# Performance work log

Measured on AMD Instinct MI355X. Metric: run time of the kernel, lower is better.

## Reference

```python
import jax, jax.numpy as jnp
import numpy as np

EMBED_DIM = 512
NUM_HEADS = 8
HEAD_DIM = EMBED_DIM // NUM_HEADS
EDGE_HIDDEN = 512
B, L = 2, 512


def setup_inputs() -> dict:
    key = jax.random.key(0)
    ks = jax.random.split(key, 16)
    s = 0.02
    inp = {
        "query": jax.random.normal(ks[0], (B, L, EMBED_DIM), jnp.float32),
        "key_in": jax.random.normal(ks[1], (B, L, EMBED_DIM), jnp.float32),
        "value": jax.random.normal(ks[2], (B, L, EMBED_DIM), jnp.float32),
        "edge_representation": jax.random.normal(ks[3], (B, L, L), jnp.float32),
        # projection weights stored as [in, out]: y = x @ W + b
        "Wq": jax.random.normal(ks[4], (EMBED_DIM, EMBED_DIM), jnp.float32) * s,
        "bq": jnp.zeros((EMBED_DIM,), jnp.float32),
        "Wk": jax.random.normal(ks[5], (EMBED_DIM, EMBED_DIM), jnp.float32) * s,
        "bk": jnp.zeros((EMBED_DIM,), jnp.float32),
        "Wv": jax.random.normal(ks[6], (EMBED_DIM, EMBED_DIM), jnp.float32) * s,
        "bv": jnp.zeros((EMBED_DIM,), jnp.float32),
        "Wo": jax.random.normal(ks[7], (EMBED_DIM, EMBED_DIM), jnp.float32) * s,
        "bo": jnp.zeros((EMBED_DIM,), jnp.float32),
        # edge MLP: Linear(1 -> 512) -> ReLU -> Linear(512 -> num_heads)
        "We1": jax.random.normal(ks[8], (1, EDGE_HIDDEN), jnp.float32) * s,
        "be1": jnp.zeros((EDGE_HIDDEN,), jnp.float32),
        "We2": jax.random.normal(ks[9], (EDGE_HIDDEN, NUM_HEADS), jnp.float32) * s,
        "be2": jnp.zeros((NUM_HEADS,), jnp.float32),
    }
    return inp


def reference(query, key_in, value, edge_representation,
              Wq, bq, Wk, bk, Wv, bv, Wo, bo, We1, be1, We2, be2):
    Bc, Lc, _ = query.shape
    # project and split heads: [B, H, L, Dh]
    def split_heads(x):
        return x.reshape(Bc, Lc, NUM_HEADS, HEAD_DIM).transpose(0, 2, 1, 3)
    Q = split_heads(query @ Wq + bq)
    K = split_heads(key_in @ Wk + bk)
    V = split_heads(value @ Wv + bv)
    # edge MLP on scalar edge features: [B, L, L, 1] -> [B, L, L, H]
    e = edge_representation[..., None]
    h = jax.nn.relu(e * We1[0] + be1)          # [B, L, L, 512]
    edge_bias = h @ We2 + be2                   # [B, L, L, H]
    scale = 1.0 / jnp.sqrt(jnp.asarray(HEAD_DIM, query.dtype))
    scores = jnp.einsum("bhqd,bhkd->bhqk", Q, K) * scale
    scores = scores + edge_bias.transpose(0, 3, 1, 2)  # [B, H, L, L]
    attn = jax.nn.softmax(scores, axis=-1)
    out = jnp.einsum("bhqk,bhkd->bhqd", attn, V)
    out = out.transpose(0, 2, 1, 3).reshape(Bc, Lc, EMBED_DIM)
    return out @ Wo + bo
```

## Files before the change

kernel.cpp:

```cpp
#include <hip/hip_runtime.h>
#include <hip/hip_bf16.h>

typedef __attribute__((ext_vector_type(8))) short bf16x8;
typedef __attribute__((ext_vector_type(4))) float f32x4;

#define LOG2E 1.44269504088896340736f

#define QB_OFF 2621440
#define KB_OFF 3145728
#define VT_OFF 3670016
#define AO_OFF 4194304
#define T_B   9437184
#define A_B   (T_B + 4096)
#define C_B   (A_B + 20480)

struct MegaArgs {
  const float *xq, *xk, *xv, *eg;
  const float *wq, *wk, *wv, *wo;
  const float *bq, *bk, *bv, *bo;
  const float *w1, *b1, *we2, *be2;
  float* out;
  unsigned short* wsb;
  float *wsT, *wsA, *wsC;
};

__device__ __forceinline__ unsigned short f2bf(float f) {
  union { __hip_bfloat16 h; unsigned short u; } c;
  c.h = __float2bfloat16(f);
  return c.u;
}

__device__ __forceinline__ uint4 pack8(float4 a, float4 b) {
  union { unsigned short us[8]; uint4 u; } r;
  r.us[0] = f2bf(a.x); r.us[1] = f2bf(a.y); r.us[2] = f2bf(a.z); r.us[3] = f2bf(a.w);
  r.us[4] = f2bf(b.x); r.us[5] = f2bf(b.y); r.us[6] = f2bf(b.z); r.us[7] = f2bf(b.w);
  return r.u;
}

__device__ void prep_block(const MegaArgs& a, char* smem) {
  float* sT   = (float*)smem;
  int*   sIdx = (int*)(smem + 2048);
  float (*sDA)[8] = (float (*)[8])(smem + 4096);
  float (*sDC)[8] = (float (*)[8])(smem + 20480);
  float* sA0 = (float*)(smem + 36864);
  float* sC0 = (float*)(smem + 36896);
  int tid = threadIdx.x, lane = tid & 63, w = tid >> 6;
  float accA[8] = {0,0,0,0,0,0,0,0}, accC[8] = {0,0,0,0,0,0,0,0};
  for (int e = 0; e < 2; ++e) {
    int p = tid + e * 256;
    float ww = a.w1[p], bb = a.b1[p];
    sT[p] = (ww != 0.f) ? (-bb / ww) : -3.4e38f;
    sIdx[p] = p;
#pragma unroll
    for (int h = 0; h < 8; ++h) {
      float w2 = a.we2[p * 8 + h];
      if (ww < 0.f)       { accA[h] += w2 * ww; accC[h] += w2 * bb; }
      else if (ww == 0.f) { accC[h] += w2 * fmaxf(bb, 0.f); }
    }
  }
  __syncthreads();
  for (int size = 2; size <= 512; size <<= 1) {
    for (int stride = size >> 1; stride > 0; stride >>= 1) {
      if (size >= 256 && stride >= 64) __syncthreads();
      else __builtin_amdgcn_wave_barrier();
      int p = tid;
      int i = ((p / stride) * (stride << 1)) + (p % stride);
      int j = i + stride;
      bool up = ((i & size) == 0);
      float ti = sT[i], tj = sT[j];
      if (up ? (ti > tj) : (ti < tj)) {
        sT[i] = tj; sT[j] = ti;
        int t = sIdx[i]; sIdx[i] = sIdx[j]; sIdx[j] = t;
      }
    }
  }
  for (int off = 32; off > 0; off >>= 1) {
#pragma unroll
    for (int h = 0; h < 8; ++h) {
      accA[h] += __shfl_xor(accA[h], off);
      accC[h] += __shfl_xor(accC[h], off);
    }
  }
  if (lane == 0) {
#pragma unroll
    for (int h = 0; h < 8; ++h) { sDA[w][h] = accA[h]; sDC[w][h] = accC[h]; }
  }
  __syncthreads();
  if (tid < 8) {
    sA0[tid] = sDA[0][tid] + sDA[1][tid] + sDA[2][tid] + sDA[3][tid];
    sC0[tid] = sDC[0][tid] + sDC[1][tid] + sDC[2][tid] + sDC[3][tid] + a.be2[tid];
  }
  __syncthreads();
  for (int e = 0; e < 2; ++e) {
    int p = tid + e * 256;
    int k = sIdx[p];
    float wk = a.w1[k], bk2 = a.b1[k];
#pragma unroll
    for (int h = 0; h < 8; ++h) {
      float w2 = a.we2[k * 8 + h];
      float da = 0.f, dc = 0.f;
      if (wk > 0.f)      { da =  w2 * wk; dc =  w2 * bk2; }
      else if (wk < 0.f) { da = -w2 * wk; dc = -w2 * bk2; }
      sDA[p][h] = da; sDC[p][h] = dc;
    }
  }
  __syncthreads();
  for (int off = 1; off < 512; off <<= 1) {
    float ra[2][8], rc[2][8];
#pragma unroll
    for (int e = 0; e < 2; ++e) {
      int p = tid + e * 256;
      if (p >= off) {
#pragma unroll
        for (int h = 0; h < 8; ++h) { ra[e][h] = sDA[p - off][h]; rc[e][h] = sDC[p - off][h]; }
      }
    }
    __syncthreads();
#pragma unroll
    for (int e = 0; e < 2; ++e) {
      int p = tid + e * 256;
      if (p >= off) {
#pragma unroll
        for (int h = 0; h < 8; ++h) { sDA[p][h] += ra[e][h]; sDC[p][h] += rc[e][h]; }
      }
    }
    __syncthreads();
  }
  bool n0 = (tid == 0) || (sT[tid] != sT[tid - 1]);
  bool n1 = (sT[tid + 256] != sT[tid + 255]);
  unsigned long long m0 = __ballot(n0), m1 = __ballot(n1);
  unsigned long long below = (1ull << lane) - 1ull;
  int loc0 = __popcll(m0 & below), loc1 = __popcll(m1 & below);
  int* tot = sIdx;
  if (lane == 0) { tot[w] = __popcll(m0); tot[4 + w] = __popcll(m1); }
  __syncthreads();
  int t[8];
#pragma unroll
  for (int j = 0; j < 8; ++j) t[j] = tot[j];
  int nuniq = t[0] + t[1] + t[2] + t[3] + t[4] + t[5] + t[6] + t[7];
  int off0 = 0, off1 = t[0] + t[1] + t[2] + t[3];
  for (int j = 0; j < 4; ++j) {
    if (j < w) { off0 += t[j]; off1 += t[4 + j]; }
  }
  if (n0) {
    int u = off0 + loc0;
    a.wsT[u] = sT[tid];
    if (tid == 0) {
#pragma unroll
      for (int h = 0; h < 8; ++h) { a.wsA[h * 513] = sA0[h]; a.wsC[h * 513] = sC0[h]; }
    } else {
#pragma unroll
      for (int h = 0; h < 8; ++h) {
        a.wsA[h * 513 + u] = sA0[h] + sDA[tid - 1][h];
        a.wsC[h * 513 + u] = sC0[h] + sDC[tid - 1][h];
      }
    }
  }
  if (n1) {
    int u = off1 + loc1;
    a.wsT[u] = sT[tid + 256];
#pragma unroll
    for (int h = 0; h < 8; ++h) {
      a.wsA[h * 513 + u] = sA0[h] + sDA[tid + 255][h];
      a.wsC[h * 513 + u] = sC0[h] + sDC[tid + 255][h];
    }
  }
  if (tid == 0) {
#pragma unroll
    for (int h = 0; h < 8; ++h) {
      a.wsA[h * 513 + nuniq] = sA0[h] + sDA[511][h];
      a.wsC[h * 513 + nuniq] = sC0[h] + sDC[511][h];
    }
    *(int*)(a.wsT + 512) = nuniq;
  }
}

__device__ void gemm_core(const float* __restrict__ Af, const unsigned short* __restrict__ Ab,
                          const float* __restrict__ W, const float* __restrict__ bias,
                          void* out, int mode, int m0, int n0, char* smem) {
  unsigned short (*sA)[72]  = (unsigned short (*)[72])smem;
  unsigned short (*sBt)[72] = (unsigned short (*)[72])(smem + 9216);
  int tid = threadIdx.x, wave = tid >> 6, lane = tid & 63;
  int quad = lane >> 4, l16 = lane & 15;
  f32x4 acc[4] = {{0.f,0.f,0.f,0.f},{0.f,0.f,0.f,0.f},{0.f,0.f,0.f,0.f},{0.f,0.f,0.f,0.f}};
  int lr = tid >> 2, ls = tid & 3;
  int kb8 = lr >> 3, klo = lr & 7;
  for (int kb = 0; kb < 512; kb += 64) {
    __syncthreads();
    if (Af) {
      const float4* ap = (const float4*)(Af + (size_t)(m0 + lr) * 512 + kb + ls * 16);
      float4 v0 = ap[0], v1 = ap[1], v2 = ap[2], v3 = ap[3];
      *(uint4*)&sA[lr][ls * 16]     = pack8(v0, v1);
      *(uint4*)&sA[lr][ls * 16 + 8] = pack8(v2, v3);
    } else {
      *(uint4*)&sA[lr][ls * 16]     = *(const uint4*)(Ab + (size_t)(m0 + lr) * 512 + kb + ls * 16);
      *(uint4*)&sA[lr][ls * 16 + 8] = *(const uint4*)(Ab + (size_t)(m0 + lr) * 512 + kb + ls * 16 + 8);
    }
    {
      const float4* wp = (const float4*)(W + (size_t)(kb + lr) * 512 + n0 + ls * 16);
      float4 w0 = wp[0], w1 = wp[1], w2 = wp[2], w3 = wp[3];
      int nb = ls * 16;
      int slot = ((kb8 ^ ls) << 3) + klo;
      sBt[nb + 0][slot] = f2bf(w0.x);  sBt[nb + 1][slot] = f2bf(w0.y);
      sBt[nb + 2][slot] = f2bf(w0.z);  sBt[nb + 3][slot] = f2bf(w0.w);
      sBt[nb + 4][slot] = f2bf(w1.x);  sBt[nb + 5][slot] = f2bf(w1.y);
      sBt[nb + 6][slot] = f2bf(w1.z);  sBt[nb + 7][slot] = f2bf(w1.w);
      sBt[nb + 8][slot] = f2bf(w2.x);  sBt[nb + 9][slot] = f2bf(w2.y);
      sBt[nb + 10][slot] = f2bf(w2.z); sBt[nb + 11][slot] = f2bf(w2.w);
      sBt[nb + 12][slot] = f2bf(w3.x); sBt[nb + 13][slot] = f2bf(w3.y);
      sBt[nb + 14][slot] = f2bf(w3.z); sBt[nb + 15][slot] = f2bf(w3.w);
    }
    __syncthreads();
    for (int ks = 0; ks < 2; ++ks) {
      bf16x8 af = *(const bf16x8*)&sA[wave * 16 + l16][ks * 32 + quad * 8];
#pragma unroll
      for (int nt = 0; nt < 4; ++nt) {
        bf16x8 bf = *(const bf16x8*)&sBt[nt * 16 + l16][((ks * 4 + quad) ^ nt) * 8];
        acc[nt] = __builtin_amdgcn_mfma_f32_16x16x32_bf16(af, bf, acc[nt], 0, 0, 0);
      }
    }
  }
  int mbase = m0 + wave * 16 + quad * 4;
#pragma unroll
  for (int nt = 0; nt < 4; ++nt) {
    int n = n0 + nt * 16 + l16;
    float bv = bias[n];
#pragma unroll
    for (int r = 0; r < 4; ++r) {
      float v = acc[nt][r] + bv;
      int m = mbase + r;
      if (mode == 0) {
        int b = m >> 9, l = m & 511, hh = n >> 6, d = n & 63;
        ((unsigned short*)out)[(((size_t)(b * 8 + hh) * 512) + l) * 64 + d] = f2bf(v);
      } else if (mode == 1) {
        ((float*)out)[(size_t)m * 512 + n] = v;
      } else {
        int b = m >> 9, l = m & 511, hh = n >> 6, d = n & 63;
        ((unsigned short*)out)[(((size_t)(b * 8 + hh) * 64) + d) * 512 + l] = f2bf(v);
      }
    }
  }
}

__device__ void attn_block(const MegaArgs& a, int qt, int h, int b, char* smem) {
  float* sT  = (float*)smem;
  float* sAh = (float*)(smem + 2048);
  float* sCh = (float*)(smem + 4100);
  unsigned short (*sP)[16][40] = (unsigned short (*)[16][40])(smem + 6160);
  float (*sO)[4][16][16] = (float (*)[4][16][16])(smem + 11280);
  float (*sM)[16] = (float (*)[16])(smem + 27664);
  float (*sL)[16] = (float (*)[16])(smem + 27920);
  const unsigned short* Qb = a.wsb + QB_OFF;
  const unsigned short* Kb = a.wsb + KB_OFF;
  const unsigned short* Vt = a.wsb + VT_OFF;
  int bh = b * 8 + h;
  int q0 = qt * 16;
  int tid = threadIdx.x, wave = tid >> 6, lane = tid & 63;
  int quad = lane >> 4, l16 = lane & 15;
  int nu = *(const int*)(a.wsT + 512);
  for (int i = tid; i < nu; i += 256) sT[i] = a.wsT[i];
  for (int i = tid; i <= nu; i += 256) { sAh[i] = a.wsA[h * 513 + i]; sCh[i] = a.wsC[h * 513 + i]; }
  const unsigned short* qp = Qb + ((size_t)bh * 512 + q0 + l16) * 64 + quad * 8;
  bf16x8 qf0 = *(const bf16x8*)qp;
  bf16x8 qf1 = *(const bf16x8*)(qp + 32);
  int key_base = wave * 128;
  f32x4 S[4][2];
#pragma unroll
  for (int kt = 0; kt < 4; ++kt) {
    int key0 = key_base + kt * 32;
#pragma unroll
    for (int half = 0; half < 2; ++half) {
      const unsigned short* kp = Kb + ((size_t)bh * 512 + key0 + half * 16 + l16) * 64 + quad * 8;
      bf16x8 kf0 = *(const bf16x8*)kp;
      bf16x8 kf1 = *(const bf16x8*)(kp + 32);
      f32x4 acc = {0.f, 0.f, 0.f, 0.f};
      acc = __builtin_amdgcn_mfma_f32_16x16x32_bf16(qf0, kf0, acc, 0, 0, 0);
      acc = __builtin_amdgcn_mfma_f32_16x16x32_bf16(qf1, kf1, acc, 0, 0, 0);
      S[kt][half] = acc;
    }
  }
  __syncthreads();
#pragma unroll
  for (int kt = 0; kt < 4; ++kt)
#pragma unroll
    for (int half = 0; half < 2; ++half)
#pragma unroll
      for (int r = 0; r < 4; ++r) {
        int eidx = (b * 512 + q0 + quad * 4 + r) * 512 + key_base + kt * 32 + half * 16 + l16;
        float ev = a.eg[eidx];
        int lo = 0, hi = nu;
        while (lo < hi) {
          int mid = (lo + hi) >> 1;
          bool c = sT[mid] < ev;
          lo = c ? mid + 1 : lo;
          hi = c ? hi : mid;
        }
        S[kt][half][r] = S[kt][half][r] * 0.125f + sAh[lo] * ev + sCh[lo];
      }
  float m_w[4], l_w[4];
#pragma unroll
  for (int r = 0; r < 4; ++r) {
    float mx = -3.4e38f;
#pragma unroll
    for (int kt = 0; kt < 4; ++kt) { mx = fmaxf(mx, fmaxf(S[kt][0][r], S[kt][1][r])); }
    for (int off = 1; off < 16; off <<= 1) mx = fmaxf(mx, __shfl_xor(mx, off, 64));
    float s = 0.f;
#pragma unroll
    for (int kt = 0; kt < 4; ++kt)
#pragma unroll
      for (int half = 0; half < 2; ++half) {
        float p = exp2f((S[kt][half][r] - mx) * LOG2E);
        S[kt][half][r] = p; s += p;
      }
    for (int off = 1; off < 16; off <<= 1) s += __shfl_xor(s, off, 64);
    m_w[r] = mx; l_w[r] = s;
  }
  f32x4 Oacc[4] = {{0.f,0.f,0.f,0.f},{0.f,0.f,0.f,0.f},{0.f,0.f,0.f,0.f},{0.f,0.f,0.f,0.f}};
#pragma unroll
  for (int kt = 0; kt < 4; ++kt) {
    int key0 = key_base + kt * 32;
#pragma unroll
    for (int half = 0; half < 2; ++half)
#pragma unroll
      for (int r = 0; r < 4; ++r)
        sP[wave][quad * 4 + r][half * 16 + l16] = f2bf(S[kt][half][r]);
    __builtin_amdgcn_wave_barrier();
    bf16x8 pf = *(const bf16x8*)&sP[wave][l16][quad * 8];
    __builtin_amdgcn_wave_barrier();
#pragma unroll
    for (int nt = 0; nt < 4; ++nt) {
      bf16x8 vf = *(const bf16x8*)(Vt + ((size_t)bh * 64 + nt * 16 + l16) * 512 + key0 + quad * 8);
      Oacc[nt] = __builtin_amdgcn_mfma_f32_16x16x32_bf16(pf, vf, Oacc[nt], 0, 0, 0);
    }
  }
  if (l16 == 0) {
#pragma unroll
    for (int r = 0; r < 4; ++r) { sM[wave][quad * 4 + r] = m_w[r]; sL[wave][quad * 4 + r] = l_w[r]; }
  }
#pragma unroll
  for (int nt = 0; nt < 4; ++nt)
#pragma unroll
    for (int r = 0; r < 4; ++r)
      sO[wave][nt][quad * 4 + r][l16] = Oacc[nt][r];
  __syncthreads();
#pragma unroll
  for (int r = 0; r < 4; ++r) {
    int row = quad * 4 + r;
    float M = fmaxf(fmaxf(sM[0][row], sM[1][row]), fmaxf(sM[2][row], sM[3][row]));
    float L = 0.f, Ov = 0.f;
#pragma unroll
    for (int wv = 0; wv < 4; ++wv) {
      float f = exp2f((sM[wv][row] - M) * LOG2E);
      L += f * sL[wv][row];
      Ov += f * sO[wv][wave][row][l16];
    }
    float v = Ov / L;
    (a.wsb + AO_OFF)[((size_t)(b * 512 + q0 + row)) * 512 + h * 64 + wave * 16 + l16] = f2bf(v);
  }
}

__global__ __launch_bounds__(256) void k1(MegaArgs a) {
  __shared__ __align__(16) char smem[36928];
  int blk = blockIdx.x;
  if (blk == 0) {
    prep_block(a, smem);
  } else {
    int g = blk - 1, z = g >> 7, rem = g & 127;
    const float* A    = (z == 0) ? a.xq : (z == 1) ? a.xk : a.xv;
    const float* W    = (z == 0) ? a.wq : (z == 1) ? a.wk : a.wv;
    const float* bias = (z == 0) ? a.bq : (z == 1) ? a.bk : a.bv;
    void* outp = (void*)(a.wsb + ((z == 0) ? QB_OFF : (z == 1) ? KB_OFF : VT_OFF));
    gemm_core(A, nullptr, W, bias, outp, (z == 2) ? 2 : 0, (rem & 15) * 64, (rem >> 4) * 64, smem);
  }
}

__global__ __launch_bounds__(256) void k2(MegaArgs a) {
  __shared__ __align__(16) char smem[28176];
  int blk = blockIdx.x;
  attn_block(a, blk & 31, (blk >> 5) & 7, blk >> 8, smem);
}

__global__ __launch_bounds__(256) void k3(MegaArgs a) {
  __shared__ __align__(16) char smem[18432];
  gemm_core(nullptr, a.wsb + AO_OFF, a.wo, a.bo, (void*)a.out, 1,
            (blockIdx.x & 15) * 64, (blockIdx.x >> 4) * 64, smem);
}

extern "C" void kernel_launch(void* const* d_in, const int* in_sizes, int n_in,
                              void* d_out, int out_size, void* d_ws, size_t ws_size,
                              hipStream_t stream) {
  MegaArgs a;
  a.xq  = (const float*)d_in[0];
  a.xk  = (const float*)d_in[1];
  a.xv  = (const float*)d_in[2];
  a.eg  = (const float*)d_in[3];
  a.wq  = (const float*)d_in[4];
  a.bq  = (const float*)d_in[5];
  a.wk  = (const float*)d_in[6];
  a.bk  = (const float*)d_in[7];
  a.wv  = (const float*)d_in[8];
  a.bv  = (const float*)d_in[9];
  a.wo  = (const float*)d_in[10];
  a.bo  = (const float*)d_in[11];
  a.w1  = (const float*)d_in[12];
  a.b1  = (const float*)d_in[13];
  a.we2 = (const float*)d_in[14];
  a.be2 = (const float*)d_in[15];
  a.out = (float*)d_out;
  a.wsb = (unsigned short*)d_ws;
  a.wsT = (float*)((char*)d_ws + T_B);
  a.wsA = (float*)((char*)d_ws + A_B);
  a.wsC = (float*)((char*)d_ws + C_B);

  k1<<<385, 256, 0, stream>>>(a);
  k2<<<512, 256, 0, stream>>>(a);
  k3<<<128, 256, 0, stream>>>(a);
}
```

Before: 137.9 us.

## Pre-convert activations and transposed weights to bf16, load GEMM tiles directly to LDS

Adds a prep kernel that converts the Q/K/V inputs to bf16 and transposes all four weight matrices into bf16 [n,k] layout in workspace. The projection GEMMs then stage tiles with global_load_lds into XOR-swizzled LDS, with no per-element conversion or scattered transposed stores in the main loop. The attention grid index mapping is also reordered so heads vary fastest. The cost is an extra kernel launch and an extra round trip of the activations and weights through global memory.

```diff
diff --git a/kernel.cpp b/kernel.cpp
--- a/kernel.cpp
+++ b/kernel.cpp
@@ -13,6 +13,8 @@
 #define T_B   9437184
 #define A_B   (T_B + 4096)
 #define C_B   (A_B + 20480)
+#define XB_OFF 8388608
+#define WT_OFF 9961472
 
 struct MegaArgs {
   const float *xq, *xk, *xv, *eg;
@@ -35,6 +37,12 @@
   r.us[0] = f2bf(a.x); r.us[1] = f2bf(a.y); r.us[2] = f2bf(a.z); r.us[3] = f2bf(a.w);
   r.us[4] = f2bf(b.x); r.us[5] = f2bf(b.y); r.us[6] = f2bf(b.z); r.us[7] = f2bf(b.w);
   return r.u;
+}
+
+__device__ __forceinline__ void gload16(const void* g, void* l) {
+  __builtin_amdgcn_global_load_lds(
+      (const __attribute__((address_space(1))) unsigned int*)g,
+      (__attribute__((address_space(3))) unsigned int*)l, 16, 0, 0);
 }
 
 __device__ void prep_block(const MegaArgs& a, char* smem) {
@@ -175,47 +183,69 @@
   }
 }
 
-__device__ void gemm_core(const float* __restrict__ Af, const unsigned short* __restrict__ Ab,
-                          const float* __restrict__ W, const float* __restrict__ bias,
-                          void* out, int mode, int m0, int n0, char* smem) {
-  unsigned short (*sA)[72]  = (unsigned short (*)[72])smem;
-  unsigned short (*sBt)[72] = (unsigned short (*)[72])(smem + 9216);
+__device__ void xconv_block(const float* __restrict__ x, unsigned short* __restrict__ xb, int j) {
+  int tid = threadIdx.x;
+  size_t base = (size_t)j * 16384;
+#pragma unroll
+  for (int it = 0; it < 8; ++it) {
+    size_t idx = base + it * 2048 + tid * 8;
+    float4 va = *(const float4*)(x + idx);
+    float4 vb = *(const float4*)(x + idx + 4);
+    *(uint4*)(xb + idx) = pack8(va, vb);
+  }
+}
+
+__device__ void wtrans_block(const float* __restrict__ W, unsigned short* __restrict__ Wt,
+                             int tile, char* smem) {
+  float (*sW)[65] = (float (*)[65])smem;
+  int tid = threadIdx.x;
+  int k0 = (tile >> 3) * 64, n0 = (tile & 7) * 64;
+  int kr = tid >> 4, c4 = (tid & 15) * 4;
+#pragma unroll
+  for (int p = 0; p < 4; ++p) {
+    int k = p * 16 + kr;
+    float4 v = *(const float4*)(W + (size_t)(k0 + k) * 512 + n0 + c4);
+    sW[k][c4] = v.x; sW[k][c4 + 1] = v.y; sW[k][c4 + 2] = v.z; sW[k][c4 + 3] = v.w;
+  }
+  __syncthreads();
+  int n = tid >> 3, kk = (tid & 7) * 8;
+#pragma unroll
+  for (int p = 0; p < 2; ++p) {
+    int nn = p * 32 + n;
+    float4 va, vb;
+    va.x = sW[kk][nn];     va.y = sW[kk + 1][nn]; va.z = sW[kk + 2][nn]; va.w = sW[kk + 3][nn];
+    vb.x = sW[kk + 4][nn]; vb.y = sW[kk + 5][nn]; vb.z = sW[kk + 6][nn]; vb.w = sW[kk + 7][nn];
+    *(uint4*)(Wt + (size_t)(n0 + nn) * 512 + k0 + kk) = pack8(va, vb);
+  }
+}
+
+__device__ void gemm_bf(const unsigned short* __restrict__ A,
+                        const unsigned short* __restrict__ Bt,
+                        const float* __restrict__ bias,
+                        void* out, int mode, int m0, int n0, char* smem) {
+  char* sA = smem;
+  char* sB = smem + 8192;
   int tid = threadIdx.x, wave = tid >> 6, lane = tid & 63;
   int quad = lane >> 4, l16 = lane & 15;
+  int lg = lane & 7, lr8 = lane >> 3;
   f32x4 acc[4] = {{0.f,0.f,0.f,0.f},{0.f,0.f,0.f,0.f},{0.f,0.f,0.f,0.f},{0.f,0.f,0.f,0.f}};
-  int lr = tid >> 2, ls = tid & 3;
-  int kb8 = lr >> 3, klo = lr & 7;
+  int swr = l16 & 7;
   for (int kb = 0; kb < 512; kb += 64) {
     __syncthreads();
-    if (Af) {
-      const float4* ap = (const float4*)(Af + (size_t)(m0 + lr) * 512 + kb + ls * 16);
-      float4 v0 = ap[0], v1 = ap[1], v2 = ap[2], v3 = ap[3];
-      *(uint4*)&sA[lr][ls * 16]     = pack8(v0, v1);
-      *(uint4*)&sA[lr][ls * 16 + 8] = pack8(v2, v3);
-    } else {
-      *(uint4*)&sA[lr][ls * 16]     = *(const uint4*)(Ab + (size_t)(m0 + lr) * 512 + kb + ls * 16);
-      *(uint4*)&sA[lr][ls * 16 + 8] = *(const uint4*)(Ab + (size_t)(m0 + lr) * 512 + kb + ls * 16 + 8);
-    }
-    {
-      const float4* wp = (const float4*)(W + (size_t)(kb + lr) * 512 + n0 + ls * 16);
-      float4 w0 = wp[0], w1 = wp[1], w2 = wp[2], w3 = wp[3];
-      int nb = ls * 16;
-      int slot = ((kb8 ^ ls) << 3) + klo;
-      sBt[nb + 0][slot] = f2bf(w0.x);  sBt[nb + 1][slot] = f2bf(w0.y);
-      sBt[nb + 2][slot] = f2bf(w0.z);  sBt[nb + 3][slot] = f2bf(w0.w);
-      sBt[nb + 4][slot] = f2bf(w1.x);  sBt[nb + 5][slot] = f2bf(w1.y);
-      sBt[nb + 6][slot] = f2bf(w1.z);  sBt[nb + 7][slot] = f2bf(w1.w);
-      sBt[nb + 8][slot] = f2bf(w2.x);  sBt[nb + 9][slot] = f2bf(w2.y);
-      sBt[nb + 10][slot] = f2bf(w2.z); sBt[nb + 11][slot] = f2bf(w2.w);
-      sBt[nb + 12][slot] = f2bf(w3.x); sBt[nb + 13][slot] = f2bf(w3.y);
-      sBt[nb + 14][slot] = f2bf(w3.z); sBt[nb + 15][slot] = f2bf(w3.w);
+#pragma unroll
+    for (int p = 0; p < 2; ++p) {
+      int row = (p * 4 + wave) * 8 + lr8;
+      int swz = (lg ^ lr8) << 3;
+      gload16(A  + (size_t)(m0 + row) * 512 + kb + swz, sA + ((p * 4 + wave) << 10));
+      gload16(Bt + (size_t)(n0 + row) * 512 + kb + swz, sB + ((p * 4 + wave) << 10));
     }
     __syncthreads();
+#pragma unroll
     for (int ks = 0; ks < 2; ++ks) {
-      bf16x8 af = *(const bf16x8*)&sA[wave * 16 + l16][ks * 32 + quad * 8];
+      bf16x8 af = *(const bf16x8*)(sA + (wave * 16 + l16) * 128 + (((ks * 4 + quad) ^ swr) << 4));
 #pragma unroll
       for (int nt = 0; nt < 4; ++nt) {
-        bf16x8 bf = *(const bf16x8*)&sBt[nt * 16 + l16][((ks * 4 + quad) ^ nt) * 8];
+        bf16x8 bf = *(const bf16x8*)(sB + (nt * 16 + l16) * 128 + (((ks * 4 + quad) ^ swr) << 4));
         acc[nt] = __builtin_amdgcn_mfma_f32_16x16x32_bf16(af, bf, acc[nt], 0, 0, 0);
       }
     }
@@ -359,31 +389,42 @@
   }
 }
 
-__global__ __launch_bounds__(256) void k1(MegaArgs a) {
+__global__ __launch_bounds__(256) void kprep(MegaArgs a) {
   __shared__ __align__(16) char smem[36928];
   int blk = blockIdx.x;
-  if (blk == 0) {
-    prep_block(a, smem);
-  } else {
-    int g = blk - 1, z = g >> 7, rem = g & 127;
-    const float* A    = (z == 0) ? a.xq : (z == 1) ? a.xk : a.xv;
-    const float* W    = (z == 0) ? a.wq : (z == 1) ? a.wk : a.wv;
-    const float* bias = (z == 0) ? a.bq : (z == 1) ? a.bk : a.bv;
-    void* outp = (void*)(a.wsb + ((z == 0) ? QB_OFF : (z == 1) ? KB_OFF : VT_OFF));
-    gemm_core(A, nullptr, W, bias, outp, (z == 2) ? 2 : 0, (rem & 15) * 64, (rem >> 4) * 64, smem);
-  }
-}
-
-__global__ __launch_bounds__(256) void k2(MegaArgs a) {
+  if (blk == 0) { prep_block(a, smem); return; }
+  if (blk <= 96) {
+    int g = blk - 1, z = g >> 5, j = g & 31;
+    const float* x = (z == 0) ? a.xq : (z == 1) ? a.xk : a.xv;
+    xconv_block(x, a.wsb + XB_OFF + (size_t)z * 524288, j);
+    return;
+  }
+  int g = blk - 97, z = g >> 6, t = g & 63;
+  const float* W = (z == 0) ? a.wq : (z == 1) ? a.wk : (z == 2) ? a.wv : a.wo;
+  wtrans_block(W, a.wsb + WT_OFF + (size_t)z * 262144, t, smem);
+}
+
+__global__ __launch_bounds__(256) void kqkv(MegaArgs a) {
+  __shared__ __align__(16) char smem[16384];
+  int blk = blockIdx.x;
+  int z = blk >> 7, rem = blk & 127;
+  const unsigned short* A  = a.wsb + XB_OFF + (size_t)z * 524288;
+  const unsigned short* Bt = a.wsb + WT_OFF + (size_t)z * 262144;
+  const float* bias = (z == 0) ? a.bq : (z == 1) ? a.bk : a.bv;
+  void* outp = (void*)(a.wsb + ((z == 0) ? QB_OFF : (z == 1) ? KB_OFF : VT_OFF));
+  gemm_bf(A, Bt, bias, outp, (z == 2) ? 2 : 0, (rem & 15) * 64, (rem >> 4) * 64, smem);
+}
+
+__global__ __launch_bounds__(256) void kattn(MegaArgs a) {
   __shared__ __align__(16) char smem[28176];
   int blk = blockIdx.x;
-  attn_block(a, blk & 31, (blk >> 5) & 7, blk >> 8, smem);
-}
-
-__global__ __launch_bounds__(256) void k3(MegaArgs a) {
-  __shared__ __align__(16) char smem[18432];
-  gemm_core(nullptr, a.wsb + AO_OFF, a.wo, a.bo, (void*)a.out, 1,
-            (blockIdx.x & 15) * 64, (blockIdx.x >> 4) * 64, smem);
+  attn_block(a, (blk >> 3) & 31, blk & 7, blk >> 8, smem);
+}
+
+__global__ __launch_bounds__(256) void kout(MegaArgs a) {
+  __shared__ __align__(16) char smem[16384];
+  gemm_bf(a.wsb + AO_OFF, a.wsb + WT_OFF + (size_t)3 * 262144, a.bo, (void*)a.out, 1,
+          (blockIdx.x & 15) * 64, (blockIdx.x >> 4) * 64, smem);
 }
 
 extern "C" void kernel_launch(void* const* d_in, const int* in_sizes, int n_in,
@@ -412,7 +453,8 @@
   a.wsA = (float*)((char*)d_ws + A_B);
   a.wsC = (float*)((char*)d_ws + C_B);
 
-  k1<<<385, 256, 0, stream>>>(a);
-  k2<<<512, 256, 0, stream>>>(a);
-  k3<<<128, 256, 0, stream>>>(a);
-}
+  kprep<<<353, 256, 0, stream>>>(a);
+  kqkv<<<384, 256, 0, stream>>>(a);
+  kattn<<<512, 256, 0, stream>>>(a);
+  kout<<<128, 256, 0, stream>>>(a);
+}
```

After: 145.3 us. 1.05x slower.

## Fuse three kernels into one persistent kernel with grid-wide barriers

Applied to the files above, without the earlier changes.

Replaces the three launches (QKV projection, attention, output projection) with one persistent kernel of 256 blocks that loops over the work of each stage and separates the stages with atomic-counter grid barriers. A memset of the barrier counters is added before the launch. The aim is to remove kernel launch gaps and tail effects between stages. In exchange each block now runs two attention tiles serially, fewer blocks run in each stage, and the spin barriers add their own cost. Correctness depends on all 256 blocks being co-resident on the GPU.

```diff
diff --git a/kernel.cpp b/kernel.cpp
--- a/kernel.cpp
+++ b/kernel.cpp
@@ -13,6 +13,8 @@
 #define T_B   9437184
 #define A_B   (T_B + 4096)
 #define C_B   (A_B + 20480)
+#define BAR_B 16777216
+#define NBLK  256
 
 struct MegaArgs {
   const float *xq, *xk, *xv, *eg;
@@ -35,6 +37,19 @@
   r.us[0] = f2bf(a.x); r.us[1] = f2bf(a.y); r.us[2] = f2bf(a.z); r.us[3] = f2bf(a.w);
   r.us[4] = f2bf(b.x); r.us[5] = f2bf(b.y); r.us[6] = f2bf(b.z); r.us[7] = f2bf(b.w);
   return r.u;
+}
+
+__device__ __forceinline__ void gbar(unsigned int* cnt) {
+  __syncthreads();
+  if (threadIdx.x == 0) {
+    __threadfence();
+    __hip_atomic_fetch_add(cnt, 1u, __ATOMIC_RELEASE, __HIP_MEMORY_SCOPE_AGENT);
+    while (__hip_atomic_load(cnt, __ATOMIC_ACQUIRE, __HIP_MEMORY_SCOPE_AGENT) < NBLK) {
+      __builtin_amdgcn_s_sleep(8);
+    }
+    __threadfence();
+  }
+  __syncthreads();
 }
 
 __device__ void prep_block(const MegaArgs& a, char* smem) {
@@ -359,31 +374,44 @@
   }
 }
 
-__global__ __launch_bounds__(256) void k1(MegaArgs a) {
+__global__ __launch_bounds__(256) void kfused(MegaArgs a) {
   __shared__ __align__(16) char smem[36928];
+  unsigned int* bar = (unsigned int*)((char*)a.wsb + BAR_B);
   int blk = blockIdx.x;
+
   if (blk == 0) {
     prep_block(a, smem);
   } else {
-    int g = blk - 1, z = g >> 7, rem = g & 127;
-    const float* A    = (z == 0) ? a.xq : (z == 1) ? a.xk : a.xv;
-    const float* W    = (z == 0) ? a.wq : (z == 1) ? a.wk : a.wv;
-    const float* bias = (z == 0) ? a.bq : (z == 1) ? a.bk : a.bv;
-    void* outp = (void*)(a.wsb + ((z == 0) ? QB_OFF : (z == 1) ? KB_OFF : VT_OFF));
-    gemm_core(A, nullptr, W, bias, outp, (z == 2) ? 2 : 0, (rem & 15) * 64, (rem >> 4) * 64, smem);
-  }
-}
-
-__global__ __launch_bounds__(256) void k2(MegaArgs a) {
-  __shared__ __align__(16) char smem[28176];
-  int blk = blockIdx.x;
-  attn_block(a, blk & 31, (blk >> 5) & 7, blk >> 8, smem);
-}
-
-__global__ __launch_bounds__(256) void k3(MegaArgs a) {
-  __shared__ __align__(16) char smem[18432];
-  gemm_core(nullptr, a.wsb + AO_OFF, a.wo, a.bo, (void*)a.out, 1,
-            (blockIdx.x & 15) * 64, (blockIdx.x >> 4) * 64, smem);
+    int g = blk - 1;
+    for (int rep = 0; rep < 2; ++rep) {
+      if (g < 384) {
+        int z = g >> 7, rem = g & 127;
+        const float* A    = (z == 0) ? a.xq : (z == 1) ? a.xk : a.xv;
+        const float* W    = (z == 0) ? a.wq : (z == 1) ? a.wk : a.wv;
+        const float* bias = (z == 0) ? a.bq : (z == 1) ? a.bk : a.bv;
+        void* outp = (void*)(a.wsb + ((z == 0) ? QB_OFF : (z == 1) ? KB_OFF : VT_OFF));
+        gemm_core(A, nullptr, W, bias, outp, (z == 2) ? 2 : 0,
+                  (rem & 15) * 64, (rem >> 4) * 64, smem);
+      }
+      g += 255;
+    }
+  }
+
+  gbar(&bar[0]);
+
+  {
+    int bh = blk >> 4, qp = blk & 15;
+    int b = bh >> 3, h = bh & 7;
+    attn_block(a, qp * 2,     h, b, smem);
+    attn_block(a, qp * 2 + 1, h, b, smem);
+  }
+
+  gbar(&bar[16]);
+
+  if (blk < 128) {
+    gemm_core(nullptr, a.wsb + AO_OFF, a.wo, a.bo, (void*)a.out, 1,
+              (blk & 15) * 64, (blk >> 4) * 64, smem);
+  }
 }
 
 extern "C" void kernel_launch(void* const* d_in, const int* in_sizes, int n_in,
@@ -412,7 +440,6 @@
   a.wsA = (float*)((char*)d_ws + A_B);
   a.wsC = (float*)((char*)d_ws + C_B);
 
-  k1<<<385, 256, 0, stream>>>(a);
-  k2<<<512, 256, 0, stream>>>(a);
-  k3<<<128, 256, 0, stream>>>(a);
-}
+  hipMemsetAsync((char*)d_ws + BAR_B, 0, 256, stream);
+  kfused<<<NBLK, 256, 0, stream>>>(a);
+}
```

After: 210.3 us. +52.5%, slower.

## Stage whole weight slab in LDS and prefetch K/V/edge fragments into registers

Applied to the files above, without the earlier changes.

The GEMM now converts and stores the full 512x64 weight slice into LDS once, behind a single barrier, and reads A fragments straight from global memory. This replaces the per-k-step loop that needed two barriers per step. In attention, the edge values, K fragments and V fragments are all loaded into registers up front so their latency overlaps with compute. P is written to LDS once for all 128 keys instead of per 32-key chunk. The cost is much larger LDS (72KB per GEMM block) and higher register pressure, which may reduce occupancy.

```diff
diff --git a/kernel.cpp b/kernel.cpp
--- a/kernel.cpp
+++ b/kernel.cpp
@@ -35,6 +35,12 @@
   r.us[0] = f2bf(a.x); r.us[1] = f2bf(a.y); r.us[2] = f2bf(a.z); r.us[3] = f2bf(a.w);
   r.us[4] = f2bf(b.x); r.us[5] = f2bf(b.y); r.us[6] = f2bf(b.z); r.us[7] = f2bf(b.w);
   return r.u;
+}
+
+__device__ __forceinline__ bf16x8 pack8v(float4 a, float4 b) {
+  union { uint4 u; bf16x8 v; } r;
+  r.u = pack8(a, b);
+  return r.v;
 }
 
 __device__ void prep_block(const MegaArgs& a, char* smem) {
@@ -175,49 +181,48 @@
   }
 }
 
-__device__ void gemm_core(const float* __restrict__ Af, const unsigned short* __restrict__ Ab,
+__device__ void gemm_fast(const float* __restrict__ Af, const unsigned short* __restrict__ Ab,
                           const float* __restrict__ W, const float* __restrict__ bias,
                           void* out, int mode, int m0, int n0, char* smem) {
-  unsigned short (*sA)[72]  = (unsigned short (*)[72])smem;
-  unsigned short (*sBt)[72] = (unsigned short (*)[72])(smem + 9216);
   int tid = threadIdx.x, wave = tid >> 6, lane = tid & 63;
   int quad = lane >> 4, l16 = lane & 15;
-  f32x4 acc[4] = {{0.f,0.f,0.f,0.f},{0.f,0.f,0.f,0.f},{0.f,0.f,0.f,0.f},{0.f,0.f,0.f,0.f}};
   int lr = tid >> 2, ls = tid & 3;
   int kb8 = lr >> 3, klo = lr & 7;
-  for (int kb = 0; kb < 512; kb += 64) {
-    __syncthreads();
+  int slot = ((kb8 ^ ls) << 3) + klo;
+#pragma unroll
+  for (int c = 0; c < 8; ++c) {
+    unsigned short (*sBt)[72] = (unsigned short (*)[72])(smem + c * 9216);
+    const float4* wp = (const float4*)(W + (size_t)(c * 64 + lr) * 512 + n0 + ls * 16);
+    float4 w0 = wp[0], w1 = wp[1], w2 = wp[2], w3 = wp[3];
+    int nb = ls * 16;
+    sBt[nb + 0][slot] = f2bf(w0.x);  sBt[nb + 1][slot] = f2bf(w0.y);
+    sBt[nb + 2][slot] = f2bf(w0.z);  sBt[nb + 3][slot] = f2bf(w0.w);
+    sBt[nb + 4][slot] = f2bf(w1.x);  sBt[nb + 5][slot] = f2bf(w1.y);
+    sBt[nb + 6][slot] = f2bf(w1.z);  sBt[nb + 7][slot] = f2bf(w1.w);
+    sBt[nb + 8][slot] = f2bf(w2.x);  sBt[nb + 9][slot] = f2bf(w2.y);
+    sBt[nb + 10][slot] = f2bf(w2.z); sBt[nb + 11][slot] = f2bf(w2.w);
+    sBt[nb + 12][slot] = f2bf(w3.x); sBt[nb + 13][slot] = f2bf(w3.y);
+    sBt[nb + 14][slot] = f2bf(w3.z); sBt[nb + 15][slot] = f2bf(w3.w);
+  }
+  __syncthreads();
+  f32x4 acc[4] = {{0.f,0.f,0.f,0.f},{0.f,0.f,0.f,0.f},{0.f,0.f,0.f,0.f},{0.f,0.f,0.f,0.f}};
+  const float*          arf = Af ? Af + (size_t)(m0 + wave * 16 + l16) * 512 : nullptr;
+  const unsigned short* arb = Ab ? Ab + (size_t)(m0 + wave * 16 + l16) * 512 : nullptr;
+#pragma unroll
+  for (int kf = 0; kf < 16; ++kf) {
+    bf16x8 af;
     if (Af) {
-      const float4* ap = (const float4*)(Af + (size_t)(m0 + lr) * 512 + kb + ls * 16);
-      float4 v0 = ap[0], v1 = ap[1], v2 = ap[2], v3 = ap[3];
-      *(uint4*)&sA[lr][ls * 16]     = pack8(v0, v1);
-      *(uint4*)&sA[lr][ls * 16 + 8] = pack8(v2, v3);
+      const float4* ap = (const float4*)(arf + kf * 32 + quad * 8);
+      af = pack8v(ap[0], ap[1]);
     } else {
-      *(uint4*)&sA[lr][ls * 16]     = *(const uint4*)(Ab + (size_t)(m0 + lr) * 512 + kb + ls * 16);
-      *(uint4*)&sA[lr][ls * 16 + 8] = *(const uint4*)(Ab + (size_t)(m0 + lr) * 512 + kb + ls * 16 + 8);
-    }
-    {
-      const float4* wp = (const float4*)(W + (size_t)(kb + lr) * 512 + n0 + ls * 16);
-      float4 w0 = wp[0], w1 = wp[1], w2 = wp[2], w3 = wp[3];
-      int nb = ls * 16;
-      int slot = ((kb8 ^ ls) << 3) + klo;
-      sBt[nb + 0][slot] = f2bf(w0.x);  sBt[nb + 1][slot] = f2bf(w0.y);
-      sBt[nb + 2][slot] = f2bf(w0.z);  sBt[nb + 3][slot] = f2bf(w0.w);
-      sBt[nb + 4][slot] = f2bf(w1.x);  sBt[nb + 5][slot] = f2bf(w1.y);
-      sBt[nb + 6][slot] = f2bf(w1.z);  sBt[nb + 7][slot] = f2bf(w1.w);
-      sBt[nb + 8][slot] = f2bf(w2.x);  sBt[nb + 9][slot] = f2bf(w2.y);
-      sBt[nb + 10][slot] = f2bf(w2.z); sBt[nb + 11][slot] = f2bf(w2.w);
-      sBt[nb + 12][slot] = f2bf(w3.x); sBt[nb + 13][slot] = f2bf(w3.y);
-      sBt[nb + 14][slot] = f2bf(w3.z); sBt[nb + 15][slot] = f2bf(w3.w);
-    }
-    __syncthreads();
-    for (int ks = 0; ks < 2; ++ks) {
-      bf16x8 af = *(const bf16x8*)&sA[wave * 16 + l16][ks * 32 + quad * 8];
-#pragma unroll
-      for (int nt = 0; nt < 4; ++nt) {
-        bf16x8 bf = *(const bf16x8*)&sBt[nt * 16 + l16][((ks * 4 + quad) ^ nt) * 8];
-        acc[nt] = __builtin_amdgcn_mfma_f32_16x16x32_bf16(af, bf, acc[nt], 0, 0, 0);
-      }
+      af = *(const bf16x8*)(arb + kf * 32 + quad * 8);
+    }
+    unsigned short (*sBt)[72] = (unsigned short (*)[72])(smem + (kf >> 1) * 9216);
+    int g = (kf & 1) * 4 + quad;
+#pragma unroll
+    for (int nt = 0; nt < 4; ++nt) {
+      bf16x8 bf = *(const bf16x8*)&sBt[nt * 16 + l16][(g ^ nt) * 8];
+      acc[nt] = __builtin_amdgcn_mfma_f32_16x16x32_bf16(af, bf, acc[nt], 0, 0, 0);
     }
   }
   int mbase = m0 + wave * 16 + quad * 4;
@@ -245,11 +250,11 @@
 __device__ void attn_block(const MegaArgs& a, int qt, int h, int b, char* smem) {
   float* sT  = (float*)smem;
   float* sAh = (float*)(smem + 2048);
-  float* sCh = (float*)(smem + 4100);
-  unsigned short (*sP)[16][40] = (unsigned short (*)[16][40])(smem + 6160);
-  float (*sO)[4][16][16] = (float (*)[4][16][16])(smem + 11280);
-  float (*sM)[16] = (float (*)[16])(smem + 27664);
-  float (*sL)[16] = (float (*)[16])(smem + 27920);
+  float* sCh = (float*)(smem + 4112);
+  unsigned short (*sP)[16][136] = (unsigned short (*)[16][136])(smem + 6176);
+  float (*sO)[4][16][16] = (float (*)[4][16][16])(smem + 23584);
+  float (*sM)[16] = (float (*)[16])(smem + 39968);
+  float (*sL)[16] = (float (*)[16])(smem + 40224);
   const unsigned short* Qb = a.wsb + QB_OFF;
   const unsigned short* Kb = a.wsb + KB_OFF;
   const unsigned short* Vt = a.wsb + VT_OFF;
@@ -260,25 +265,40 @@
   int nu = *(const int*)(a.wsT + 512);
   for (int i = tid; i < nu; i += 256) sT[i] = a.wsT[i];
   for (int i = tid; i <= nu; i += 256) { sAh[i] = a.wsA[h * 513 + i]; sCh[i] = a.wsC[h * 513 + i]; }
+  int key_base = wave * 128;
+  float egv[4][2][4];
+#pragma unroll
+  for (int kt = 0; kt < 4; ++kt)
+#pragma unroll
+    for (int half = 0; half < 2; ++half)
+#pragma unroll
+      for (int r = 0; r < 4; ++r) {
+        int eidx = (b * 512 + q0 + quad * 4 + r) * 512 + key_base + kt * 32 + half * 16 + l16;
+        egv[kt][half][r] = a.eg[eidx];
+      }
   const unsigned short* qp = Qb + ((size_t)bh * 512 + q0 + l16) * 64 + quad * 8;
   bf16x8 qf0 = *(const bf16x8*)qp;
   bf16x8 qf1 = *(const bf16x8*)(qp + 32);
-  int key_base = wave * 128;
+  bf16x8 kfr[4][2][2];
+#pragma unroll
+  for (int kt = 0; kt < 4; ++kt)
+#pragma unroll
+    for (int half = 0; half < 2; ++half) {
+      const unsigned short* kp =
+          Kb + ((size_t)bh * 512 + key_base + kt * 32 + half * 16 + l16) * 64 + quad * 8;
+      kfr[kt][half][0] = *(const bf16x8*)kp;
+      kfr[kt][half][1] = *(const bf16x8*)(kp + 32);
+    }
   f32x4 S[4][2];
 #pragma unroll
-  for (int kt = 0; kt < 4; ++kt) {
-    int key0 = key_base + kt * 32;
+  for (int kt = 0; kt < 4; ++kt)
 #pragma unroll
     for (int half = 0; half < 2; ++half) {
-      const unsigned short* kp = Kb + ((size_t)bh * 512 + key0 + half * 16 + l16) * 64 + quad * 8;
-      bf16x8 kf0 = *(const bf16x8*)kp;
-      bf16x8 kf1 = *(const bf16x8*)(kp + 32);
       f32x4 acc = {0.f, 0.f, 0.f, 0.f};
-      acc = __builtin_amdgcn_mfma_f32_16x16x32_bf16(qf0, kf0, acc, 0, 0, 0);
-      acc = __builtin_amdgcn_mfma_f32_16x16x32_bf16(qf1, kf1, acc, 0, 0, 0);
+      acc = __builtin_amdgcn_mfma_f32_16x16x32_bf16(qf0, kfr[kt][half][0], acc, 0, 0, 0);
+      acc = __builtin_amdgcn_mfma_f32_16x16x32_bf16(qf1, kfr[kt][half][1], acc, 0, 0, 0);
       S[kt][half] = acc;
     }
-  }
   __syncthreads();
 #pragma unroll
   for (int kt = 0; kt < 4; ++kt)
@@ -286,8 +306,7 @@
     for (int half = 0; half < 2; ++half)
 #pragma unroll
       for (int r = 0; r < 4; ++r) {
-        int eidx = (b * 512 + q0 + quad * 4 + r) * 512 + key_base + kt * 32 + half * 16 + l16;
-        float ev = a.eg[eidx];
+        float ev = egv[kt][half][r];
         int lo = 0, hi = nu;
         while (lo < hi) {
           int mid = (lo + hi) >> 1;
@@ -297,6 +316,13 @@
         }
         S[kt][half][r] = S[kt][half][r] * 0.125f + sAh[lo] * ev + sCh[lo];
       }
+  bf16x8 vfr[4][4];
+#pragma unroll
+  for (int kt = 0; kt < 4; ++kt)
+#pragma unroll
+    for (int nt = 0; nt < 4; ++nt)
+      vfr[kt][nt] = *(const bf16x8*)(Vt + ((size_t)bh * 64 + nt * 16 + l16) * 512 +
+                                     key_base + kt * 32 + quad * 8);
   float m_w[4], l_w[4];
 #pragma unroll
   for (int r = 0; r < 4; ++r) {
@@ -315,23 +341,21 @@
     for (int off = 1; off < 16; off <<= 1) s += __shfl_xor(s, off, 64);
     m_w[r] = mx; l_w[r] = s;
   }
+#pragma unroll
+  for (int kt = 0; kt < 4; ++kt)
+#pragma unroll
+    for (int half = 0; half < 2; ++half)
+#pragma unroll
+      for (int r = 0; r < 4; ++r)
+        sP[wave][quad * 4 + r][kt * 32 + half * 16 + l16] = f2bf(S[kt][half][r]);
+  __builtin_amdgcn_wave_barrier();
   f32x4 Oacc[4] = {{0.f,0.f,0.f,0.f},{0.f,0.f,0.f,0.f},{0.f,0.f,0.f,0.f},{0.f,0.f,0.f,0.f}};
 #pragma unroll
   for (int kt = 0; kt < 4; ++kt) {
-    int key0 = key_base + kt * 32;
-#pragma unroll
-    for (int half = 0; half < 2; ++half)
-#pragma unroll
-      for (int r = 0; r < 4; ++r)
-        sP[wave][quad * 4 + r][half * 16 + l16] = f2bf(S[kt][half][r]);
-    __builtin_amdgcn_wave_barrier();
-    bf16x8 pf = *(const bf16x8*)&sP[wave][l16][quad * 8];
-    __builtin_amdgcn_wave_barrier();
-#pragma unroll
-    for (int nt = 0; nt < 4; ++nt) {
-      bf16x8 vf = *(const bf16x8*)(Vt + ((size_t)bh * 64 + nt * 16 + l16) * 512 + key0 + quad * 8);
-      Oacc[nt] = __builtin_amdgcn_mfma_f32_16x16x32_bf16(pf, vf, Oacc[nt], 0, 0, 0);
-    }
+    bf16x8 pf = *(const bf16x8*)&sP[wave][l16][kt * 32 + quad * 8];
+#pragma unroll
+    for (int nt = 0; nt < 4; ++nt)
+      Oacc[nt] = __builtin_amdgcn_mfma_f32_16x16x32_bf16(pf, vfr[kt][nt], Oacc[nt], 0, 0, 0);
   }
   if (l16 == 0) {
 #pragma unroll
@@ -359,8 +383,8 @@
   }
 }
 
-__global__ __launch_bounds__(256) void k1(MegaArgs a) {
-  __shared__ __align__(16) char smem[36928];
+__global__ __launch_bounds__(256, 2) void k1(MegaArgs a) {
+  __shared__ __align__(16) char smem[73728];
   int blk = blockIdx.x;
   if (blk == 0) {
     prep_block(a, smem);
@@ -370,19 +394,19 @@
     const float* W    = (z == 0) ? a.wq : (z == 1) ? a.wk : a.wv;
     const float* bias = (z == 0) ? a.bq : (z == 1) ? a.bk : a.bv;
     void* outp = (void*)(a.wsb + ((z == 0) ? QB_OFF : (z == 1) ? KB_OFF : VT_OFF));
-    gemm_core(A, nullptr, W, bias, outp, (z == 2) ? 2 : 0, (rem & 15) * 64, (rem >> 4) * 64, smem);
-  }
-}
-
-__global__ __launch_bounds__(256) void k2(MegaArgs a) {
-  __shared__ __align__(16) char smem[28176];
+    gemm_fast(A, nullptr, W, bias, outp, (z == 2) ? 2 : 0, (rem & 15) * 64, (rem >> 4) * 64, smem);
+  }
+}
+
+__global__ __launch_bounds__(256, 2) void k2(MegaArgs a) {
+  __shared__ __align__(16) char smem[40480];
   int blk = blockIdx.x;
   attn_block(a, blk & 31, (blk >> 5) & 7, blk >> 8, smem);
 }
 
-__global__ __launch_bounds__(256) void k3(MegaArgs a) {
-  __shared__ __align__(16) char smem[18432];
-  gemm_core(nullptr, a.wsb + AO_OFF, a.wo, a.bo, (void*)a.out, 1,
+__global__ __launch_bounds__(256, 2) void k3(MegaArgs a) {
+  __shared__ __align__(16) char smem[73728];
+  gemm_fast(nullptr, a.wsb + AO_OFF, a.wo, a.bo, (void*)a.out, 1,
             (blockIdx.x & 15) * 64, (blockIdx.x >> 4) * 64, smem);
 }
 
```

After: 134.9 us. 1.02x faster.
